# Kernel tuning notes

Hardware: AMD Instinct MI355X
Metric: run time of the kernel (lower is better)

## Reference

```python
import jax, jax.numpy as jnp
import numpy as np


def pairwise_distances(x):
    # x: [N, D] -> squared euclidean distances [N, N], clamped at 0
    sq = jnp.sum(x * x, axis=1)  # [N]
    dist = sq[:, None] + sq[None, :] - 2.0 * (x @ x.T)
    return jnp.maximum(dist, 0.0)


def setup_inputs() -> dict:
    key = jax.random.key(0)
    k1, k2 = jax.random.split(key)
    N, D, T = 8192, 128, 200000
    x = jax.random.normal(k1, (N, D), dtype=jnp.float32)
    triplets = jax.random.randint(k2, (T, 3), 0, N, dtype=jnp.int64)
    return {"x": x, "triplets": triplets}


def reference(x, triplets):
    dist = pairwise_distances(x)  # [N, N]
    i, j, k = triplets[:, 0], triplets[:, 1], triplets[:, 2]
    d_ij = dist[i, j]  # [T] anchor-positive distances
    d_ik = dist[i, k]  # [T] anchor-negative distances
    # loss = mean over triplets of log(1 + exp(d_ij - d_ik)) (uniform weights)
    loss = jnp.mean(jnp.log1p(jnp.exp(d_ij - d_ik)))
    return loss
```

## Files before the change

### kernel.cpp

```cpp
#include <hip/hip_runtime.h>
#include <math.h>

#define TRIP_BLOCKS 2048


template<int CTRL>
__device__ __forceinline__ float dpp_shr_add(float v) {
    int m = __builtin_amdgcn_update_dpp(0, __float_as_int(v), CTRL, 0xf, 0xf, true);
    return v + __int_as_float(m);
}

__device__ __forceinline__ float row16_sum(float v) {
    v = dpp_shr_add<0x111>(v);
    v = dpp_shr_add<0x112>(v);
    v = dpp_shr_add<0x114>(v);
    v = dpp_shr_add<0x118>(v);
    return v;
}

__device__ __forceinline__ float softplus_fast(float z) {
    float u = __expf(-fabsf(z));
    return fmaxf(z, 0.0f) + __logf(1.0f + u);
}

__device__ __forceinline__ void sq_diff(const float4 a, const float4 b, float& acc) {
    float t;
    t = a.x - b.x; acc = fmaf(t, t, acc);
    t = a.y - b.y; acc = fmaf(t, t, acc);
    t = a.z - b.z; acc = fmaf(t, t, acc);
    t = a.w - b.w; acc = fmaf(t, t, acc);
}

__global__ void __launch_bounds__(256)
trip_kernel(const float* __restrict__ x, const int* __restrict__ trip,
            float* __restrict__ partial, int T) {
    const int lane    = threadIdx.x & 63;
    const int sub     = threadIdx.x & 15;
    const int gid     = (blockIdx.x * blockDim.x + threadIdx.x) >> 4;
    const int ngroups = (TRIP_BLOCKS * 256) >> 4;

    const float4* xv = (const float4*)x;

    float local = 0.0f;

    int n = gid;
    int i = 0, j = 0, k = 0;
    if (n < T) {
        i = trip[3 * n];
        j = trip[3 * n + 1];
        k = trip[3 * n + 2];
    }
    while (n < T) {
        float4 a0 = xv[i * 32 + sub], a1 = xv[i * 32 + sub + 16];
        float4 b0 = xv[j * 32 + sub], b1 = xv[j * 32 + sub + 16];
        float4 c0 = xv[k * 32 + sub], c1 = xv[k * 32 + sub + 16];

        int n2 = n + ngroups;
        if (n2 < T) {
            i = trip[3 * n2];
            j = trip[3 * n2 + 1];
            k = trip[3 * n2 + 2];
        }

        float d1 = 0.0f, d2 = 0.0f;
        sq_diff(a0, b0, d1); sq_diff(a1, b1, d1);
        sq_diff(a0, c0, d2); sq_diff(a1, c1, d2);

        d1 = row16_sum(d1);
        d2 = row16_sum(d2);
        if (sub == 15)
            local += softplus_fast(d1 - d2);

        n = n2;
    }

    local += __shfl_xor(local, 16, 64);
    local += __shfl_xor(local, 32, 64);

    __shared__ float wsum[4];
    int wid = threadIdx.x >> 6;
    if (lane == 15) wsum[wid] = local;
    __syncthreads();
    if (threadIdx.x == 0)
        partial[blockIdx.x] = wsum[0] + wsum[1] + wsum[2] + wsum[3];
}

__global__ void __launch_bounds__(256)
finalize_kernel(const float* __restrict__ partial, int nparts,
                float* __restrict__ out, int T) {
    float s = 0.0f;
    for (int idx = threadIdx.x; idx < nparts; idx += 256)
        s += partial[idx];
#pragma unroll
    for (int off = 32; off; off >>= 1) s += __shfl_xor(s, off, 64);
    __shared__ float wsum[4];
    int wid = threadIdx.x >> 6;
    if ((threadIdx.x & 63) == 0) wsum[wid] = s;
    __syncthreads();
    if (threadIdx.x == 0)
        out[0] = (wsum[0] + wsum[1] + wsum[2] + wsum[3]) / (float)T;
}

extern "C" void kernel_launch(void* const* d_in, const int* in_sizes, int n_in,
                              void* d_out, int out_size, void* d_ws, size_t ws_size,
                              hipStream_t stream) {
    const float* x    = (const float*)d_in[0];
    const int*   trip = (const int*)d_in[1];
    float*       out  = (float*)d_out;

    int T = in_sizes[1] / 3;

    float* partial = (float*)d_ws;

    trip_kernel<<<TRIP_BLOCKS, 256, 0, stream>>>(x, trip, partial, T);
    finalize_kernel<<<1, 256, 0, stream>>>(partial, TRIP_BLOCKS, out, T);
}
```

Measured before the change: 74.54 us.

## Assign one triplet per wavefront and reduce the distance difference across the wave

Each wavefront of 64 lanes now handles one triplet, with each lane loading a float2 from each of the three rows. Previously a 16-lane group handled one triplet using two float4 loads per row. The two squared distances are folded into a single difference before a full-wave DPP reduction, which adds row_bcast steps. Triplet indices become wave-uniform via readfirstlane, so they can be fetched with scalar loads. In exchange, each wave has fewer loads in flight, there are more loop iterations per wave, and every triplet pays for a longer reduction.

```diff
diff --git a/kernel.cpp b/kernel.cpp
--- a/kernel.cpp
+++ b/kernel.cpp
@@ -4,17 +4,19 @@
 #define TRIP_BLOCKS 2048
 
 
-template<int CTRL>
-__device__ __forceinline__ float dpp_shr_add(float v) {
-    int m = __builtin_amdgcn_update_dpp(0, __float_as_int(v), CTRL, 0xf, 0xf, true);
+template<int CTRL, int ROWMASK>
+__device__ __forceinline__ float dpp_add(float v) {
+    int m = __builtin_amdgcn_update_dpp(0, __float_as_int(v), CTRL, ROWMASK, 0xf, true);
     return v + __int_as_float(m);
 }
 
-__device__ __forceinline__ float row16_sum(float v) {
-    v = dpp_shr_add<0x111>(v);
-    v = dpp_shr_add<0x112>(v);
-    v = dpp_shr_add<0x114>(v);
-    v = dpp_shr_add<0x118>(v);
+__device__ __forceinline__ float wave64_sum(float v) {
+    v = dpp_add<0x111, 0xf>(v);
+    v = dpp_add<0x112, 0xf>(v);
+    v = dpp_add<0x114, 0xf>(v);
+    v = dpp_add<0x118, 0xf>(v);
+    v = dpp_add<0x142, 0xa>(v);
+    v = dpp_add<0x143, 0xc>(v);
     return v;
 }
 
@@ -23,63 +25,54 @@
     return fmaxf(z, 0.0f) + __logf(1.0f + u);
 }
 
-__device__ __forceinline__ void sq_diff(const float4 a, const float4 b, float& acc) {
-    float t;
-    t = a.x - b.x; acc = fmaf(t, t, acc);
-    t = a.y - b.y; acc = fmaf(t, t, acc);
-    t = a.z - b.z; acc = fmaf(t, t, acc);
-    t = a.w - b.w; acc = fmaf(t, t, acc);
-}
-
 __global__ void __launch_bounds__(256)
 trip_kernel(const float* __restrict__ x, const int* __restrict__ trip,
             float* __restrict__ partial, int T) {
-    const int lane    = threadIdx.x & 63;
-    const int sub     = threadIdx.x & 15;
-    const int gid     = (blockIdx.x * blockDim.x + threadIdx.x) >> 4;
-    const int ngroups = (TRIP_BLOCKS * 256) >> 4;
+    const int lane   = threadIdx.x & 63;
+    const int wid    = threadIdx.x >> 6;
+    const int gwave  = (blockIdx.x * blockDim.x + threadIdx.x) >> 6;
+    const int nwaves = (TRIP_BLOCKS * 256) >> 6;
 
-    const float4* xv = (const float4*)x;
+    const float2* xv = (const float2*)x;
 
     float local = 0.0f;
 
-    int n = gid;
+    int n = gwave;
     int i = 0, j = 0, k = 0;
     if (n < T) {
-        i = trip[3 * n];
-        j = trip[3 * n + 1];
-        k = trip[3 * n + 2];
+        int n0 = __builtin_amdgcn_readfirstlane(n);
+        i = trip[3 * n0];
+        j = trip[3 * n0 + 1];
+        k = trip[3 * n0 + 2];
     }
     while (n < T) {
-        float4 a0 = xv[i * 32 + sub], a1 = xv[i * 32 + sub + 16];
-        float4 b0 = xv[j * 32 + sub], b1 = xv[j * 32 + sub + 16];
-        float4 c0 = xv[k * 32 + sub], c1 = xv[k * 32 + sub + 16];
+        float2 a = xv[(size_t)i * 64 + lane];
+        float2 b = xv[(size_t)j * 64 + lane];
+        float2 c = xv[(size_t)k * 64 + lane];
 
-        int n2 = n + ngroups;
+        int n2 = n + nwaves;
         if (n2 < T) {
-            i = trip[3 * n2];
-            j = trip[3 * n2 + 1];
-            k = trip[3 * n2 + 2];
+            int n0 = __builtin_amdgcn_readfirstlane(n2);
+            i = trip[3 * n0];
+            j = trip[3 * n0 + 1];
+            k = trip[3 * n0 + 2];
         }
 
-        float d1 = 0.0f, d2 = 0.0f;
-        sq_diff(a0, b0, d1); sq_diff(a1, b1, d1);
-        sq_diff(a0, c0, d2); sq_diff(a1, c1, d2);
+        float t1 = a.x - b.x, t2 = a.x - c.x;
+        float e  = t1 * t1;
+        e = fmaf(-t2, t2, e);
+        t1 = a.y - b.y; t2 = a.y - c.y;
+        e = fmaf(t1, t1, e);
+        e = fmaf(-t2, t2, e);
 
-        d1 = row16_sum(d1);
-        d2 = row16_sum(d2);
-        if (sub == 15)
-            local += softplus_fast(d1 - d2);
-
+        e = wave64_sum(e);
+        if (lane == 63)
+            local += softplus_fast(e);
         n = n2;
     }
 
-    local += __shfl_xor(local, 16, 64);
-    local += __shfl_xor(local, 32, 64);
-
     __shared__ float wsum[4];
-    int wid = threadIdx.x >> 6;
-    if (lane == 15) wsum[wid] = local;
+    if (lane == 63) wsum[wid] = local;
     __syncthreads();
     if (threadIdx.x == 0)
         partial[blockIdx.x] = wsum[0] + wsum[1] + wsum[2] + wsum[3];
```

New measurement: 79.70 us. +6.9%, slower.
